# Kernel optimization log

Measured on AMD Instinct MI355X. Metric: run time of the kernel, lower is better.

Reference implementation:

```python
import jax, jax.numpy as jnp
import numpy as np

VOCAB, H, B, S = 30522, 768, 32, 512


def setup_inputs() -> dict:
    key = jax.random.key(0)
    ks = jax.random.split(key, 12)
    inp = {
        'hiddens': jax.random.normal(ks[0], (B, S, H), dtype=jnp.float32),
        'input_ids': jax.random.randint(ks[1], (B, S), 0, VOCAB, dtype=jnp.int32),
        'in_table': jax.random.bernoulli(ks[2], 0.5, (VOCAB,)),
        'table': jax.random.normal(ks[3], (VOCAB, H), dtype=jnp.float32) * 0.05,
        'W1m': jax.random.normal(ks[4], (512, H), dtype=jnp.float32) * 0.03,
        'b1m': jnp.zeros((512,), jnp.float32),
        'W2m': jax.random.normal(ks[5], (H, 512), dtype=jnp.float32) * 0.03,
        'b2m': jnp.zeros((H,), jnp.float32),
        'Wa1': jax.random.normal(ks[6], (100, H), dtype=jnp.float32) * 0.03,
        'ba1': jnp.zeros((100,), jnp.float32),
        'Wa2': jax.random.normal(ks[7], (1, 100), dtype=jnp.float32) * 0.1,
        'ba2': jnp.zeros((1,), jnp.float32),
        'Wl': jax.random.normal(ks[8], (3, 2 * H), dtype=jnp.float32) * 0.02,
        'bl': jnp.zeros((3,), jnp.float32),
    }
    return inp


def reference(hiddens, input_ids, in_table, table, W1m, b1m, W2m, b2m,
              Wa1, ba1, Wa2, ba2, Wl, bl):
    # --- vectorized replacement of the per-token dict lookup + MLP2 loops ---
    # gather knowledge vectors for every token: [B,S,768]
    know = table[input_ids]
    # MLP2 up to X2 (only X2 is used downstream): 768 -> 512 -> 768, relu twice
    x = jax.nn.relu(jnp.einsum('bsh,kh->bsk', know, W1m) + b1m)   # [B,S,512]
    fine = jax.nn.relu(jnp.einsum('bsk,hk->bsh', x, W2m) + b2m)   # [B,S,768]
    # membership mask; position 0 (CLS) is never looked up in the loop
    pos = jnp.arange(input_ids.shape[1])[None, :]                 # [1,S]
    mask = in_table[input_ids] & (pos > 0)                        # [B,S] bool
    m = mask[..., None].astype(hiddens.dtype)
    # wordhiddens: fine vector where token in table else zeros
    wordhiddens = fine * m                                        # [B,S,768]
    # --- StructuredSelfAttention over wordhiddens[:, 1:] ---
    wh = wordhiddens[:, 1:]                                       # [B,S-1,768]
    a = jnp.tanh(jnp.einsum('bsh,ah->bsa', wh, Wa1) + ba1)        # [B,S-1,100]
    a = jnp.einsum('bsa,oa->bso', a, Wa2) + ba2                   # [B,S-1,1]
    attn = jax.nn.softmax(a, axis=1)                              # softmax over seq
    sent = jnp.einsum('bso,bsh->boh', attn, wh)                   # [B,1,768]
    cls_knowledge = jnp.sum(sent, axis=1)                         # r=1, [B,768]
    # --- classifier head (method='ce'; dropout in eval mode = identity) ---
    cls_feats = jnp.concatenate([hiddens[:, 0, :], cls_knowledge], axis=1)  # [B,1536]
    predicts = cls_feats @ Wl.T + bl                              # [B,3]
    return predicts
```

## Files before the change

### kernel.cpp

```cpp
#include <hip/hip_runtime.h>
#include <stdint.h>
#include <math.h>

#define B_ 32
#define S_ 512
#define H_ 768
#define V_ 30522
#define M_ (B_*S_)
#define N1_ 512

typedef __attribute__((ext_vector_type(8))) short bf16x8;
typedef __attribute__((ext_vector_type(4))) float f32x4;

__device__ __forceinline__ float bf2f(unsigned short u){
  union { unsigned int u; float f; } c; c.u = ((unsigned int)u)<<16; return c.f;
}
__device__ __forceinline__ unsigned short f2bf(float f){
  union { float f; unsigned int u; } c; c.f=f;
  unsigned int u = c.u + 0x7FFFu + ((c.u>>16)&1u);
  return (unsigned short)(u>>16);
}
__device__ __forceinline__ bool tbl_get(const void* t, int id, int flag){
  if(flag==1) return ((const int*)t)[id]!=0;
  if(flag==2) return ((const unsigned int*)t)[id]!=0u;
  return ((const unsigned char*)t)[id]!=0;
}
__device__ __forceinline__ void gload_lds16(const void* g, void* l){
  __builtin_amdgcn_global_load_lds(
    (const __attribute__((address_space(1))) void*)g,
    (__attribute__((address_space(3))) void*)l, 16, 0, 0);
}

__global__ __launch_bounds__(256) void k_prep(const void* __restrict__ in_table,
  const int* __restrict__ ids,
  const float* __restrict__ W1, const float* __restrict__ W2,
  const float* __restrict__ Wa1, const float* __restrict__ Wa2, const float* __restrict__ ba1,
  unsigned short* __restrict__ W1bf, unsigned short* __restrict__ W2bf,
  unsigned short* __restrict__ Wa1bf, float* __restrict__ Wa2p, float* __restrict__ ba1p,
  int* __restrict__ cid, int* __restrict__ cnt, float* __restrict__ out)
{
  const int blk = blockIdx.x;
  const int t = threadIdx.x;
  if(blk < 32){
    __shared__ int sh[512];
    __shared__ int sflag;
    if(t < 64){
      const int v = ((const int*)in_table)[t];
      const unsigned int u = (unsigned int)v;
      const unsigned long long b01 = __ballot(v==0 || v==1);
      const unsigned long long bfl = __ballot(u==0u || u==0x3F800000u);
      if(t==0) sflag = (~b01==0ull) ? 1 : ((~bfl==0ull) ? 2 : 0);
    }
    __syncthreads();
    const int flag = sflag;
    const int m0 = blk*S_ + t, m1 = m0 + 256;
    const int id0 = ids[m0], id1 = ids[m1];
    const int mk0 = ((t!=0) && tbl_get(in_table, id0, flag)) ? 1 : 0;
    const int mk1 = tbl_get(in_table, id1, flag) ? 1 : 0;
    sh[t] = mk0; sh[t+256] = mk1;
    __syncthreads();
    for(int off=1; off<512; off<<=1){
      const int a0 = (t >= off) ? sh[t-off] : 0;
      const int a1 = (t+256 >= off) ? sh[t+256-off] : 0;
      __syncthreads();
      sh[t] += a0; sh[t+256] += a1;
      __syncthreads();
    }
    const int total = sh[511];
    const int r0 = sh[t] - mk0;
    const int r1 = sh[t+256] - mk1;
    if(t >= total)     cid[blk*S_ + t]       = 0;
    if(t+256 >= total) cid[blk*S_ + t + 256] = 0;
    if(mk0) cid[blk*S_ + r0] = id0;
    if(mk1) cid[blk*S_ + r1] = id1;
    if(t==0) cnt[blk] = total;
  } else {
    if(blk == 32 && t < 96) out[t] = 0.f;
    const int g = (blk-32)*256 + t, st = (gridDim.x-32)*256;
    for(int i=g;i<512*H_;i+=st) W1bf[i]=f2bf(W1[i]);
    for(int i=g;i<H_*512;i+=st) W2bf[i]=f2bf(W2[i]);
    for(int i=g;i<128*H_;i+=st) Wa1bf[i] = (i<100*H_)? f2bf(Wa1[i]) : (unsigned short)0;
    if(g < 128){ Wa2p[g] = (g<100)? Wa2[g] : 0.f; ba1p[g] = (g<100)? ba1[g] : 0.f; }
  }
}

__global__ __launch_bounds__(256) void k_gemm1g(
  const float* __restrict__ table, const int* __restrict__ cid,
  const unsigned short* __restrict__ Bw, const float* __restrict__ bias,
  const int* __restrict__ cnt, unsigned short* __restrict__ C)
{
  const int m0 = blockIdx.x << 7;
  if((m0 & (S_-1)) >= cnt[m0 >> 9]) return;
  __shared__ __align__(16) float AsF[2][128*32];
  __shared__ __align__(16) unsigned short Bs[2][128*32];
  const int tid = threadIdx.x;
  const int lane = tid & 63;
  const int wave = tid >> 6;
  const int wr = wave >> 1, wc = wave & 1;
  const int n0 = blockIdx.y << 7;

  const float* gaq[4];
  #pragma unroll
  for(int q=0;q<4;q++){
    const int s = q*256 + tid;
    const int row = s >> 3, ch = s & 7;
    const int sch = ch ^ (row & 7);
    gaq[q] = table + (size_t)cid[m0 + row]*H_ + (sch<<2);
  }
  const int f0 = tid, f1 = 256 + tid;
  const int r0 = f0 >> 2, s0 = ((f0 & 3) ^ ((f0 >> 3) & 3)) << 3;
  const int r1 = f1 >> 2, s1 = ((f1 & 3) ^ ((f1 >> 3) & 3)) << 3;
  const unsigned short* gb0 = Bw + (size_t)(n0 + r0)*H_ + s0;
  const unsigned short* gb1 = Bw + (size_t)(n0 + r1)*H_ + s1;

  f32x4 acc[4][4] = {};
  const int arow = (wr<<6) + (lane & 15);
  const int brow = (wc<<6) + (lane & 15);
  const int kg = lane >> 4;
  const int slb = ((kg ^ ((lane>>1)&3)) << 3);

  auto STAGE = [&](int buf, int k0){
    #pragma unroll
    for(int q=0;q<4;q++)
      gload_lds16(gaq[q] + k0, AsF[buf] + (q*256 + tid)*4);
    gload_lds16(gb0 + k0, Bs[buf] + (wave<<9));
    gload_lds16(gb1 + k0, Bs[buf] + 2048 + (wave<<9));
  };
  auto COMPUTE = [&](int buf){
    bf16x8 a[4], b[4];
    #pragma unroll
    for(int m=0;m<4;m++){
      const int R = arow + (m<<4);
      const int c1 = (2*kg) ^ (R&7), c2 = (2*kg+1) ^ (R&7);
      const f32x4 fa = *(const f32x4*)(AsF[buf] + R*32 + (c1<<2));
      const f32x4 fb = *(const f32x4*)(AsF[buf] + R*32 + (c2<<2));
      union { float f; unsigned int u; } z0,z1,z2,z3,z4,z5,z6,z7;
      z0.f=fa.x; z1.f=fa.y; z2.f=fa.z; z3.f=fa.w;
      z4.f=fb.x; z5.f=fb.y; z6.f=fb.z; z7.f=fb.w;
      union { unsigned int w[4]; bf16x8 v; } cv;
      cv.w[0] = (z1.u & 0xFFFF0000u) | (z0.u >> 16);
      cv.w[1] = (z3.u & 0xFFFF0000u) | (z2.u >> 16);
      cv.w[2] = (z5.u & 0xFFFF0000u) | (z4.u >> 16);
      cv.w[3] = (z7.u & 0xFFFF0000u) | (z6.u >> 16);
      a[m] = cv.v;
    }
    #pragma unroll
    for(int n=0;n<4;n++) b[n] = *(const bf16x8*)(Bs[buf] + (brow + (n<<4))*32 + slb);
    #pragma unroll
    for(int m=0;m<4;m++)
      #pragma unroll
      for(int n=0;n<4;n++)
        acc[m][n] = __builtin_amdgcn_mfma_f32_16x16x32_bf16(a[m], b[n], acc[m][n], 0,0,0);
  };

  STAGE(0, 0);
  __syncthreads();
  for(int k0 = 0; k0 < H_; k0 += 64){
    if(k0+32 < H_) STAGE(1, k0+32);
    COMPUTE(0);
    __syncthreads();
    if(k0+64 < H_) STAGE(0, k0+64);
    COMPUTE(1);
    __syncthreads();
  }

  const int crow0 = (lane>>4) << 2;
  const int ccol  = lane & 15;
  float bia[4];
  #pragma unroll
  for(int n=0;n<4;n++) bia[n] = bias[n0 + (wc<<6) + (n<<4) + ccol];
  #pragma unroll
  for(int m=0;m<4;m++){
    const int gr0 = m0 + (wr<<6) + (m<<4) + crow0;
    #pragma unroll
    for(int j=0;j<4;j++){
      const size_t rbase = (size_t)(gr0 + j) * N1_;
      #pragma unroll
      for(int n=0;n<4;n++){
        float v = acc[m][n][j] + bia[n];
        v = fmaxf(v, 0.f);
        C[rbase + n0 + (wc<<6) + (n<<4) + ccol] = f2bf(v);
      }
    }
  }
}

template<int KTOT, int NTOT>
__global__ __launch_bounds__(256) void k_gemm(
  const unsigned short* __restrict__ A, const unsigned short* __restrict__ Bw,
  const float* __restrict__ bias, const int* __restrict__ cnt,
  unsigned short* __restrict__ C)
{
  const int m0 = blockIdx.x << 7;
  if((m0 & (S_-1)) >= cnt[m0 >> 9]) return;
  __shared__ __align__(16) unsigned short As[2][128*32];
  __shared__ __align__(16) unsigned short Bs[2][128*32];
  const int tid = threadIdx.x;
  const int lane = tid & 63;
  const int wave = tid >> 6;
  const int wr = wave >> 1, wc = wave & 1;
  const int n0 = blockIdx.y << 7;

  const int f0 = tid, f1 = 256 + tid;
  const int r0 = f0 >> 2, s0 = ((f0 & 3) ^ ((f0 >> 3) & 3)) << 3;
  const int r1 = f1 >> 2, s1 = ((f1 & 3) ^ ((f1 >> 3) & 3)) << 3;
  const unsigned short* ga0 = A + (size_t)(m0 + r0)*KTOT + s0;
  const unsigned short* ga1 = A + (size_t)(m0 + r1)*KTOT + s1;
  const unsigned short* gb0 = Bw + (size_t)(n0 + r0)*KTOT + s0;
  const unsigned short* gb1 = Bw + (size_t)(n0 + r1)*KTOT + s1;

  f32x4 acc[4][4] = {};
  const int arow = (wr<<6) + (lane & 15);
  const int brow = (wc<<6) + (lane & 15);
  const int sl   = (((lane>>4) ^ ((lane>>1)&3)) << 3);

  auto STAGE = [&](int buf, int k0){
    gload_lds16(ga0 + k0, As[buf] + (wave<<9));
    gload_lds16(ga1 + k0, As[buf] + 2048 + (wave<<9));
    gload_lds16(gb0 + k0, Bs[buf] + (wave<<9));
    gload_lds16(gb1 + k0, Bs[buf] + 2048 + (wave<<9));
  };
  auto COMPUTE = [&](int buf){
    bf16x8 a[4], b[4];
    #pragma unroll
    for(int m=0;m<4;m++) a[m] = *(const bf16x8*)(As[buf] + (arow + (m<<4))*32 + sl);
    #pragma unroll
    for(int n=0;n<4;n++) b[n] = *(const bf16x8*)(Bs[buf] + (brow + (n<<4))*32 + sl);
    #pragma unroll
    for(int m=0;m<4;m++)
      #pragma unroll
      for(int n=0;n<4;n++)
        acc[m][n] = __builtin_amdgcn_mfma_f32_16x16x32_bf16(a[m], b[n], acc[m][n], 0,0,0);
  };

  STAGE(0, 0);
  __syncthreads();
  for(int k0 = 0; k0 < KTOT; k0 += 64){
    if(k0+32 < KTOT) STAGE(1, k0+32);
    COMPUTE(0);
    __syncthreads();
    if(k0+64 < KTOT) STAGE(0, k0+64);
    COMPUTE(1);
    __syncthreads();
  }

  const int crow0 = (lane>>4) << 2;
  const int ccol  = lane & 15;
  float bia[4];
  #pragma unroll
  for(int n=0;n<4;n++) bia[n] = bias[n0 + (wc<<6) + (n<<4) + ccol];
  #pragma unroll
  for(int m=0;m<4;m++){
    const int gr0 = m0 + (wr<<6) + (m<<4) + crow0;
    #pragma unroll
    for(int j=0;j<4;j++){
      const size_t rbase = (size_t)(gr0 + j) * NTOT;
      #pragma unroll
      for(int n=0;n<4;n++){
        float v = acc[m][n][j] + bia[n];
        v = fmaxf(v, 0.f);
        C[rbase + n0 + (wc<<6) + (n<<4) + ccol] = f2bf(v);
      }
    }
  }
}

__global__ __launch_bounds__(256) void k_score(
  const unsigned short* __restrict__ A, const unsigned short* __restrict__ Bw,
  const float* __restrict__ ba1p, const float* __restrict__ Wa2p, const float* __restrict__ ba2,
  const int* __restrict__ cnt, float* __restrict__ scoresC)
{
  const int m0 = blockIdx.x << 5;
  if((m0 & (S_-1)) >= cnt[m0 >> 9]) return;
  __shared__ __align__(16) unsigned short As[2][32*32];
  __shared__ __align__(16) unsigned short Bs[2][128*32];
  __shared__ float sums[32][4];
  const int tid = threadIdx.x;
  const int lane = tid & 63;
  const int wave = tid >> 6;

  const int fa = tid, ra = fa >> 2, sa = ((fa & 3) ^ ((fa >> 3) & 3)) << 3;
  const unsigned short* gaS = A + (size_t)(m0 + ra)*H_ + sa;
  const int f0 = tid, f1 = 256 + tid;
  const int r0 = f0 >> 2, s0 = ((f0 & 3) ^ ((f0 >> 3) & 3)) << 3;
  const int r1 = f1 >> 2, s1 = ((f1 & 3) ^ ((f1 >> 3) & 3)) << 3;
  const unsigned short* gb0 = Bw + (size_t)r0*H_ + s0;
  const unsigned short* gb1 = Bw + (size_t)r1*H_ + s1;

  f32x4 acc[2][2] = {};
  const int sl = (((lane>>4) ^ ((lane>>1)&3)) << 3);

  auto STAGE = [&](int buf, int k0){
    if(wave < 2) gload_lds16(gaS + k0, As[buf] + (wave<<9));
    gload_lds16(gb0 + k0, Bs[buf] + (wave<<9));
    gload_lds16(gb1 + k0, Bs[buf] + 2048 + (wave<<9));
  };
  auto COMPUTE = [&](int buf){
    bf16x8 a[2], b[2];
    #pragma unroll
    for(int m=0;m<2;m++) a[m] = *(const bf16x8*)(As[buf] + ((lane&15) + (m<<4))*32 + sl);
    #pragma unroll
    for(int n=0;n<2;n++) b[n] = *(const bf16x8*)(Bs[buf] + ((wave<<5) + (n<<4) + (lane&15))*32 + sl);
    #pragma unroll
    for(int m=0;m<2;m++)
      #pragma unroll
      for(int n=0;n<2;n++)
        acc[m][n] = __builtin_amdgcn_mfma_f32_16x16x32_bf16(a[m], b[n], acc[m][n], 0,0,0);
  };

  STAGE(0, 0);
  __syncthreads();
  for(int k0 = 0; k0 < H_; k0 += 64){
    if(k0+32 < H_) STAGE(1, k0+32);
    COMPUTE(0);
    __syncthreads();
    if(k0+64 < H_) STAGE(0, k0+64);
    COMPUTE(1);
    __syncthreads();
  }

  float ps[2][4] = {{0.f,0.f,0.f,0.f},{0.f,0.f,0.f,0.f}};
  #pragma unroll
  for(int n=0;n<2;n++){
    const int c = (wave<<5) + (n<<4) + (lane & 15);
    const float w2 = Wa2p[c], bb = ba1p[c];
    #pragma unroll
    for(int m=0;m<2;m++)
      #pragma unroll
      for(int j=0;j<4;j++)
        ps[m][j] = fmaf(tanhf(acc[m][n][j] + bb), w2, ps[m][j]);
  }
  #pragma unroll
  for(int msk=1; msk<16; msk<<=1)
    #pragma unroll
    for(int m=0;m<2;m++)
      #pragma unroll
      for(int j=0;j<4;j++)
        ps[m][j] += __shfl_xor(ps[m][j], msk, 64);
  if((lane & 15) == 0){
    #pragma unroll
    for(int m=0;m<2;m++)
      #pragma unroll
      for(int j=0;j<4;j++)
        sums[(m<<4) + ((lane>>4)<<2) + j][wave] = ps[m][j];
  }
  __syncthreads();
  if(tid < 32)
    scoresC[m0 + tid] = sums[tid][0] + sums[tid][1] + sums[tid][2] + sums[tid][3] + ba2[0];
}

__global__ __launch_bounds__(256) void k_tail(
  const float* __restrict__ scoresC, const int* __restrict__ cnt,
  const unsigned short* __restrict__ wh, const float* __restrict__ hiddens,
  const float* __restrict__ Wa2, const float* __restrict__ ba1, const float* __restrict__ ba2,
  const float* __restrict__ Wl, const float* __restrict__ bl,
  float* __restrict__ out)
{
  const int b = blockIdx.x >> 4, ch = blockIdx.x & 15, tid = threadIdx.x;
  const int n = cnt[b];
  const int j0 = ch << 5;
  const int nch = min(n - j0, 32);
  __shared__ float red[256];

  if(ch == 0){
    const float* hid = hiddens + (size_t)b * S_ * H_;
    for(int c=0;c<3;c++){
      float p = 0.f;
      #pragma unroll
      for(int r=0;r<3;r++){
        const int h = tid + (r<<8);
        p = fmaf(hid[h], Wl[c*1536 + h], p);
      }
      red[tid]=p; __syncthreads();
      for(int st=128; st>0; st>>=1){ if(tid<st) red[tid]+=red[tid+st]; __syncthreads(); }
      if(tid==0) atomicAdd(out + b*3 + c, red[0] + bl[c]);
      __syncthreads();
    }
  }
  if(nch <= 0) return;

  __shared__ float sw[32];
  red[tid] = (tid < 100) ? Wa2[tid]*tanhf(ba1[tid]) : 0.f;
  __syncthreads();
  for(int st=128; st>0; st>>=1){ if(tid<st) red[tid]+=red[tid+st]; __syncthreads(); }
  const float c0 = red[0] + ba2[0];
  __syncthreads();
  const float s1 = (tid     < n) ? scoresC[b*S_ + tid      ] : -1e30f;
  const float s2 = (tid+256 < n) ? scoresC[b*S_ + tid + 256] : -1e30f;
  float lm = fmaxf(s1, s2);
  if(tid==0 && n < 511) lm = fmaxf(lm, c0);
  red[tid] = lm; __syncthreads();
  for(int st=128; st>0; st>>=1){ if(tid<st) red[tid]=fmaxf(red[tid], red[tid+st]); __syncthreads(); }
  const float mx = red[0]; __syncthreads();
  const float e1 = (tid     < n) ? __expf(s1-mx) : 0.f;
  const float e2 = (tid+256 < n) ? __expf(s2-mx) : 0.f;
  red[tid] = e1+e2; __syncthreads();
  for(int st=128; st>0; st>>=1){ if(tid<st) red[tid]+=red[tid+st]; __syncthreads(); }
  const float denom = red[0] + (float)(511 - n) * __expf(c0 - mx);
  const float inv = 1.f/denom;
  if(tid < 32){
    const int j = j0 + tid;
    sw[tid] = (j < n) ? __expf(scoresC[b*S_+j]-mx)*inv : 0.f;
  }
  __syncthreads();

  float a0=0.f, a1=0.f, a2=0.f, a3=0.f;
  if(tid < 192){
    const unsigned short* wp = wh + ((size_t)(b*S_ + j0))*H_ + (tid<<2);
    #pragma unroll 4
    for(int t=0;t<nch;t++){
      const float wv = sw[t];
      const ushort4 v = *(const ushort4*)(wp + (size_t)t*H_);
      a0 = fmaf(wv, bf2f(v.x), a0);
      a1 = fmaf(wv, bf2f(v.y), a1);
      a2 = fmaf(wv, bf2f(v.z), a2);
      a3 = fmaf(wv, bf2f(v.w), a3);
    }
  }
  for(int c=0;c<3;c++){
    float p = 0.f;
    if(tid < 192){
      const float4 wl = *(const float4*)(Wl + c*1536 + 768 + (tid<<2));
      p = a0*wl.x + a1*wl.y + a2*wl.z + a3*wl.w;
    }
    red[tid]=p; __syncthreads();
    for(int st=128; st>0; st>>=1){ if(tid<st) red[tid]+=red[tid+st]; __syncthreads(); }
    if(tid==0) atomicAdd(out + b*3 + c, red[0]);
    __syncthreads();
  }
}

extern "C" void kernel_launch(void* const* d_in, const int* in_sizes, int n_in,
                              void* d_out, int out_size, void* d_ws, size_t ws_size,
                              hipStream_t stream)
{
  const float* hiddens = (const float*)d_in[0];
  const int*   ids     = (const int*)d_in[1];
  const void*  in_tab  = d_in[2];
  const float* table   = (const float*)d_in[3];
  const float* W1      = (const float*)d_in[4];
  const float* b1      = (const float*)d_in[5];
  const float* W2      = (const float*)d_in[6];
  const float* b2      = (const float*)d_in[7];
  const float* Wa1     = (const float*)d_in[8];
  const float* ba1     = (const float*)d_in[9];
  const float* Wa2     = (const float*)d_in[10];
  const float* ba2     = (const float*)d_in[11];
  const float* Wl      = (const float*)d_in[12];
  const float* bl      = (const float*)d_in[13];
  float* out = (float*)d_out;

  char* w = (char*)d_ws;
  unsigned short* wh    = (unsigned short*)w;
  unsigned short* x     = (unsigned short*)(w + 25165824);
  unsigned short* W1bf  = (unsigned short*)(w + 41943040);
  unsigned short* W2bf  = (unsigned short*)(w + 42729472);
  unsigned short* Wa1bf = (unsigned short*)(w + 43515904);
  float* Wa2p    = (float*)(w + 43712512);
  float* ba1p    = (float*)(w + 43713024);
  float* scoresC = (float*)(w + 43713536);
  int*   cid     = (int*)  (w + 43779072);
  int*   cnt     = (int*)  (w + 43844608);

  hipLaunchKernelGGL(k_prep,   dim3(768), dim3(256), 0, stream, in_tab, ids,
                     W1, W2, Wa1, Wa2, ba1, W1bf, W2bf, Wa1bf, Wa2p, ba1p, cid, cnt, out);
  hipLaunchKernelGGL(k_gemm1g, dim3(128, 4), dim3(256), 0, stream, table, cid, W1bf, b1, cnt, x);
  hipLaunchKernelGGL((k_gemm<N1_, H_>), dim3(128, 6), dim3(256), 0, stream, x, W2bf, b2, cnt, wh);
  hipLaunchKernelGGL(k_score,  dim3(512), dim3(256), 0, stream, wh, Wa1bf, ba1p, Wa2p, ba2, cnt, scoresC);
  hipLaunchKernelGGL(k_tail,   dim3(512), dim3(256), 0, stream, scoresC, cnt, wh, hiddens, Wa2, ba1, ba2, Wl, bl, out);
}
```

Before: 78.34 us.

## Triple-buffer GEMM K-loop with explicit vmcnt waits and raw barriers

Both GEMM kernels move from a double-buffered LDS pipeline with __syncthreads to a three-stage ring that keeps two tile loads in flight. Explicit s_waitcnt vmcnt counts make each wave wait only for the tile it is about to compute. The aim is to hide global-load latency behind MFMA work. In exchange, LDS use grows by half, which may lower occupancy, and the hand-set vmcnt numbers must match the exact count of memory ops per stage or the pipeline races.

Measured after the change: 82.71 us. +5.6%, slower.

```diff
diff --git a/kernel.cpp b/kernel.cpp
--- a/kernel.cpp
+++ b/kernel.cpp
@@ -91,8 +91,8 @@
 {
   const int m0 = blockIdx.x << 7;
   if((m0 & (S_-1)) >= cnt[m0 >> 9]) return;
-  __shared__ __align__(16) float AsF[2][128*32];
-  __shared__ __align__(16) unsigned short Bs[2][128*32];
+  __shared__ __align__(16) float AsF[3][128*32];
+  __shared__ __align__(16) unsigned short Bs[3][128*32];
   const int tid = threadIdx.x;
   const int lane = tid & 63;
   const int wave = tid >> 6;
@@ -153,15 +153,18 @@
         acc[m][n] = __builtin_amdgcn_mfma_f32_16x16x32_bf16(a[m], b[n], acc[m][n], 0,0,0);
   };
 
+  const int NT = H_/32;
   STAGE(0, 0);
-  __syncthreads();
-  for(int k0 = 0; k0 < H_; k0 += 64){
-    if(k0+32 < H_) STAGE(1, k0+32);
-    COMPUTE(0);
-    __syncthreads();
-    if(k0+64 < H_) STAGE(0, k0+64);
-    COMPUTE(1);
-    __syncthreads();
+  STAGE(1, 32);
+  for(int t=0; t<NT; ++t){
+    const int tn = t+2;
+    if(tn < NT) STAGE(tn%3, tn*32);
+    if(t+2 < NT)      asm volatile("s_waitcnt vmcnt(12)" ::: "memory");
+    else if(t+1 < NT) asm volatile("s_waitcnt vmcnt(6)"  ::: "memory");
+    else              asm volatile("s_waitcnt vmcnt(0)"  ::: "memory");
+    __builtin_amdgcn_s_barrier();
+    COMPUTE(t%3);
+    __builtin_amdgcn_s_barrier();
   }
 
   const int crow0 = (lane>>4) << 2;
@@ -193,8 +196,8 @@
 {
   const int m0 = blockIdx.x << 7;
   if((m0 & (S_-1)) >= cnt[m0 >> 9]) return;
-  __shared__ __align__(16) unsigned short As[2][128*32];
-  __shared__ __align__(16) unsigned short Bs[2][128*32];
+  __shared__ __align__(16) unsigned short As[3][128*32];
+  __shared__ __align__(16) unsigned short Bs[3][128*32];
   const int tid = threadIdx.x;
   const int lane = tid & 63;
   const int wave = tid >> 6;
@@ -233,15 +236,18 @@
         acc[m][n] = __builtin_amdgcn_mfma_f32_16x16x32_bf16(a[m], b[n], acc[m][n], 0,0,0);
   };
 
+  const int NT = KTOT/32;
   STAGE(0, 0);
-  __syncthreads();
-  for(int k0 = 0; k0 < KTOT; k0 += 64){
-    if(k0+32 < KTOT) STAGE(1, k0+32);
-    COMPUTE(0);
-    __syncthreads();
-    if(k0+64 < KTOT) STAGE(0, k0+64);
-    COMPUTE(1);
-    __syncthreads();
+  STAGE(1, 32);
+  for(int t=0; t<NT; ++t){
+    const int tn = t+2;
+    if(tn < NT) STAGE(tn%3, tn*32);
+    if(t+2 < NT)      asm volatile("s_waitcnt vmcnt(8)" ::: "memory");
+    else if(t+1 < NT) asm volatile("s_waitcnt vmcnt(4)" ::: "memory");
+    else              asm volatile("s_waitcnt vmcnt(0)" ::: "memory");
+    __builtin_amdgcn_s_barrier();
+    COMPUTE(t%3);
+    __builtin_amdgcn_s_barrier();
   }
 
   const int crow0 = (lane>>4) << 2;
```
